# Performance work log

Measured on AMD Instinct MI355X. Metric: run time of the kernel, lower is better.

Reference implementation:

```python
import jax, jax.numpy as jnp
import numpy as np

B, S, D_IN, D_Q, D_V, H = 2, 2048, 1024, 1024, 1024, 16
HD_Q, HD_V = D_Q // H, D_V // H
SCALE = float(D_Q) ** 0.5  # source scales by sqrt(d_q), NOT sqrt(head_dim)


def setup_inputs() -> dict:
    key = jax.random.key(0)
    k1, k2, k3, k4, k5 = jax.random.split(key, 5)
    return {
        "x": jax.random.normal(k1, (B, S, D_IN), dtype=jnp.float32),
        "w_q": jax.random.normal(k2, (D_IN, D_Q), dtype=jnp.float32),
        "w_k": jax.random.normal(k3, (D_IN, D_Q), dtype=jnp.float32),
        "w_v": jax.random.normal(k4, (D_IN, D_V), dtype=jnp.float32),
        "W_o": jax.random.normal(k5, (D_IN, D_V), dtype=jnp.float32),
    }


def reference(x, w_q, w_k, w_v, W_o):
    b, s, _ = x.shape
    # projections: [b, s, d]
    q = x @ w_q
    k = x @ w_k
    v = x @ w_v
    # split heads -> [b, h, s, hd]
    Q = q.reshape(b, s, H, HD_Q).transpose(0, 2, 1, 3)
    K = k.reshape(b, s, H, HD_Q).transpose(0, 2, 1, 3)
    V = v.reshape(b, s, H, HD_V).transpose(0, 2, 1, 3)
    # full [b, h, s, s] score matrix (naive attention, as in source)
    scores = jnp.einsum("bhqd,bhkd->bhqk", Q, K)
    # FAITHFUL QUIRK: source applies softmax over dim=0 (batch axis)
    attn = jax.nn.softmax(scores / SCALE, axis=0)
    vals = jnp.einsum("bhqk,bhkd->bhqd", attn, V)
    vals = vals.transpose(0, 2, 1, 3).reshape(b, s, D_V)
    return vals @ W_o
```

## Files before the change

kernel.cpp:

```cpp
#include <hip/hip_runtime.h>


typedef _Float16 f16;
typedef __attribute__((ext_vector_type(8))) _Float16 f16x8;
typedef __attribute__((ext_vector_type(4))) _Float16 f16x4;
typedef __attribute__((ext_vector_type(4))) float f32x4;

#define MFMA16(a,b,c) __builtin_amdgcn_mfma_f32_16x16x32_f16(a,b,c,0,0,0)
#define GLD16(gp, lp) __builtin_amdgcn_global_load_lds(                         \
    (const __attribute__((address_space(1))) void*)(gp),                        \
    (__attribute__((address_space(3))) void*)(lp), 16, 0, 0)

__global__ __launch_bounds__(256) void convert_x(const float* __restrict__ x,
                                                 f16* __restrict__ xh, int n4) {
    int i = blockIdx.x * 256 + threadIdx.x;
    if (i >= n4) return;
    float4 v = ((const float4*)x)[i];
    f16x4 h;
    h[0] = (f16)v.x; h[1] = (f16)v.y; h[2] = (f16)v.z; h[3] = (f16)v.w;
    *(f16x4*)(xh + (long)i * 4) = h;
}

__global__ __launch_bounds__(256) void transpose_w(const float* __restrict__ w0, const float* __restrict__ w1,
                                                   const float* __restrict__ w2, const float* __restrict__ w3,
                                                   f16* __restrict__ o0, f16* __restrict__ o1,
                                                   f16* __restrict__ o2, f16* __restrict__ o3) {
    const float* w; f16* o;
    switch (blockIdx.z) {
        case 0: w = w0; o = o0; break;
        case 1: w = w1; o = o1; break;
        case 2: w = w2; o = o2; break;
        default: w = w3; o = o3; break;
    }
    __shared__ alignas(16) f16 t[64][72];
    const int tid = threadIdx.x;
    const int d0 = blockIdx.x * 64, j0 = blockIdx.y * 64;
    #pragma unroll
    for (int it = 0; it < 4; ++it) {
        int idx = it * 256 + tid;
        int row = idx >> 4, c4 = idx & 15;
        float4 v = *(const float4*)(w + (long)(d0 + row) * 1024 + j0 + c4 * 4);
        f16x4 h;
        h[0] = (f16)v.x; h[1] = (f16)v.y; h[2] = (f16)v.z; h[3] = (f16)v.w;
        *(f16x4*)&t[row][c4 * 4] = h;
    }
    __syncthreads();
    #pragma unroll
    for (int it = 0; it < 4; ++it) {
        int idx = it * 256 + tid;
        int jr = idx >> 4, d4 = idx & 15;
        f16x4 h;
        #pragma unroll
        for (int m = 0; m < 4; ++m) h[m] = t[d4 * 4 + m][jr];
        *(f16x4*)(o + (long)(j0 + jr) * 1024 + d0 + d4 * 4) = h;
    }
}

__global__ __launch_bounds__(256, 1) void gemm_qkv(const f16* __restrict__ A,
                                                   const f16* __restrict__ Wt,
                                                   f16* __restrict__ Qg,
                                                   f16* __restrict__ Kg,
                                                   f16* __restrict__ Vtg) {
    __shared__ alignas(16) f16 smem[16384];
    f16* As = smem;
    f16* Bs = smem + 8192;
    const int tid = threadIdx.x;
    const int wave = tid >> 6, lane = tid & 63;
    const int l15 = lane & 15, lq = lane >> 4;
    const int sw = l15 & 7;
    const int m0 = blockIdx.x * 128, n0 = blockIdx.y * 128;
    const int wr = (wave >> 1) * 64, wc = (wave & 1) * 64;
    const int r8 = lane >> 3;
    const int swc8 = ((lane & 7) ^ r8) * 8;

    f32x4 acc[4][4] = {};

    for (int kt = 0; kt < 16; ++kt) {
        __syncthreads();
        #pragma unroll
        for (int i = 0; i < 4; ++i) {
            GLD16(A  + (long)(m0 + wave * 32 + i * 8 + r8) * 1024 + kt * 64 + swc8, As + (wave * 32 + i * 8) * 64);
            GLD16(Wt + (long)(n0 + wave * 32 + i * 8 + r8) * 1024 + kt * 64 + swc8, Bs + (wave * 32 + i * 8) * 64);
        }
        __syncthreads();
        #pragma unroll
        for (int s2 = 0; s2 < 2; ++s2) {
            const int rc = ((s2 * 4 + lq) ^ sw) << 3;
            f16x8 af[4], bf[4];
            #pragma unroll
            for (int i = 0; i < 4; ++i) af[i] = *(const f16x8*)&As[(wr + i * 16 + l15) * 64 + rc];
            #pragma unroll
            for (int j = 0; j < 4; ++j) bf[j] = *(const f16x8*)&Bs[(wc + j * 16 + l15) * 64 + rc];
            #pragma unroll
            for (int i = 0; i < 4; ++i)
                #pragma unroll
                for (int j = 0; j < 4; ++j)
                    acc[i][j] = MFMA16(af[i], bf[j], acc[i][j]);
        }
    }

    const int sel = n0 >> 10;
    const int nb = n0 - (sel << 10);

    if (sel < 2) {
        f16* dst = sel == 0 ? Qg : Kg;
        const float qs = sel == 0 ? 0.045084219f : 1.0f;
        __syncthreads();
        #pragma unroll
        for (int i = 0; i < 4; ++i)
            #pragma unroll
            for (int j = 0; j < 4; ++j) {
                int row0 = wr + i * 16 + lq * 4;
                int colb = wc + j * 16 + l15;
                int chunk = colb >> 3, sub = colb & 7;
                #pragma unroll
                for (int r = 0; r < 4; ++r) {
                    int row = row0 + r;
                    smem[row * 128 + ((chunk ^ (row & 7)) << 3) + sub] = (f16)(acc[i][j][r] * qs);
                }
            }
        __syncthreads();
        #pragma unroll
        for (int e = 0; e < 8; ++e) {
            int id = e * 256 + tid;
            int row = id >> 4, c = id & 15;
            f16x8 v = *(const f16x8*)&smem[row * 128 + ((c ^ (row & 7)) << 3)];
            int gr = m0 + row, b = gr >> 11, s = gr & 2047;
            int gc = nb + c * 8, hh = gc >> 6, hd = gc & 63;
            *(f16x8*)(dst + (long)((b * 16 + hh) * 2048 + s) * 64 + hd) = v;
        }
    } else {
        #pragma unroll
        for (int i = 0; i < 4; ++i)
            #pragma unroll
            for (int j = 0; j < 4; ++j) {
                int gr0 = m0 + wr + i * 16 + lq * 4;
                int gc  = nb + wc + j * 16 + l15;
                int b = gr0 >> 11, s = gr0 & 2047;
                int hh = gc >> 6, hd = gc & 63;
                f16x4 v;
                #pragma unroll
                for (int r = 0; r < 4; ++r) v[r] = (f16)acc[i][j][r];
                *(f16x4*)(Vtg + (long)((b * 16 + hh) * 64 + hd) * 2048 + s) = v;
            }
    }
}

__global__ __launch_bounds__(256, 1) void gemm_out(const f16* __restrict__ A0,
                                                   const f16* __restrict__ A1,
                                                   const f16* __restrict__ Bt,
                                                   float* __restrict__ outp) {
    __shared__ alignas(16) f16 As[64][72];
    __shared__ alignas(16) f16 Bs[128][64];
    const int tid = threadIdx.x;
    const int wave = tid >> 6, lane = tid & 63;
    const int l15 = lane & 15, lq = lane >> 4;
    const int sw = l15 & 7;
    const int m0 = blockIdx.x * 64, n0 = blockIdx.y * 128;
    const int wr = (wave >> 1) * 32, wc = (wave & 1) * 64;
    const int r8 = lane >> 3;
    const int swc8 = ((lane & 7) ^ r8) * 8;

    f32x4 acc[2][4] = {};

    for (int kt = 0; kt < 16; ++kt) {
        __syncthreads();
        #pragma unroll
        for (int it = 0; it < 2; ++it) {
            int idx = it * 256 + tid;
            int row = idx >> 3, c = idx & 7;
            f16x8 a = *(const f16x8*)(A0 + (long)(m0 + row) * 1024 + kt * 64 + c * 8)
                    + *(const f16x8*)(A1 + (long)(m0 + row) * 1024 + kt * 64 + c * 8);
            *(f16x8*)&As[row][c * 8] = a;
        }
        #pragma unroll
        for (int i = 0; i < 4; ++i)
            GLD16(Bt + (long)(n0 + wave * 32 + i * 8 + r8) * 1024 + kt * 64 + swc8, &Bs[wave * 32 + i * 8][0]);
        __syncthreads();
        #pragma unroll
        for (int s2 = 0; s2 < 2; ++s2) {
            const int rc = ((s2 * 4 + lq) ^ sw) << 3;
            f16x8 af[2], bf[4];
            #pragma unroll
            for (int i = 0; i < 2; ++i) af[i] = *(const f16x8*)&As[wr + i * 16 + l15][s2 * 32 + lq * 8];
            #pragma unroll
            for (int j = 0; j < 4; ++j) bf[j] = *(const f16x8*)&Bs[wc + j * 16 + l15][rc];
            #pragma unroll
            for (int i = 0; i < 2; ++i)
                #pragma unroll
                for (int j = 0; j < 4; ++j)
                    acc[i][j] = MFMA16(af[i], bf[j], acc[i][j]);
        }
    }

    #pragma unroll
    for (int i = 0; i < 2; ++i)
        #pragma unroll
        for (int j = 0; j < 4; ++j) {
            int gr0 = m0 + wr + i * 16 + lq * 4;
            int gc  = n0 + wc + j * 16 + l15;
            #pragma unroll
            for (int r = 0; r < 4; ++r)
                outp[(long)(gr0 + r) * 1024 + gc] = acc[i][j][r];
        }
}

__global__ __launch_bounds__(128, 2) void attention_kernel(const f16* __restrict__ Qg,
                                                           const f16* __restrict__ Kg,
                                                           const f16* __restrict__ Vtg,
                                                           f16* __restrict__ vals0,
                                                           f16* __restrict__ vals1) {
    __shared__ alignas(16) f16 Ks [2][64][64];
    __shared__ alignas(16) f16 Vts[2][64][64];
    __shared__ alignas(16) f16 Ps [2][32][64];
    const int tid = threadIdx.x;
    const int wave = tid >> 6, lane = tid & 63;
    const int l15 = lane & 15, lq = lane >> 4;
    const int sw = l15 & 7;

    const int bid = blockIdx.x;
    const int xcd = bid & 7, sl = bid >> 3;
    const int h  = xcd * 2 + (sl & 1);
    const int qt = (sl >> 1) & 31, ks = sl >> 6;
    const int q0 = qt * 64, kt0 = ks * 16;
    f16* vals = ks ? vals1 : vals0;
    const int qr = q0 + wave * 32;

    f16x8 qfr[2][2][2];
    #pragma unroll
    for (int b2 = 0; b2 < 2; ++b2)
        #pragma unroll
        for (int qq = 0; qq < 2; ++qq)
            #pragma unroll
            for (int s2 = 0; s2 < 2; ++s2)
                qfr[b2][qq][s2] = *(const f16x8*)(Qg + (long)((b2 * 16 + h) * 2048 + qr + qq * 16 + l15) * 64
                                                  + s2 * 32 + lq * 8);

    f32x4 acc[2][2][4] = {};

    const int r8 = lane >> 3;
    const int swc8 = ((lane & 7) ^ r8) * 8;
    const f16* kb0 = Kg  + (long)(h * 2048 + kt0 * 64) * 64 + r8 * 64 + swc8;
    const f16* kb1 = kb0 + (long)16 * 2048 * 64;
    const f16* vb0 = Vtg + (long)(h * 64 + r8) * 2048 + kt0 * 64 + swc8;
    const f16* vb1 = vb0 + (long)16 * 64 * 2048;

    for (int kt = 0; kt < 16; ++kt) {
        __syncthreads();
        if (wave == 0) {
            const f16* g0 = kb0 + kt * 4096;
            const f16* g1 = kb1 + kt * 4096;
            #pragma unroll
            for (int i = 0; i < 8; ++i) GLD16(g0 + i * 512, &Ks[0][0][0] + i * 512);
            #pragma unroll
            for (int i = 0; i < 8; ++i) GLD16(g1 + i * 512, &Ks[1][0][0] + i * 512);
        } else {
            const f16* g0 = vb0 + kt * 64;
            const f16* g1 = vb1 + kt * 64;
            #pragma unroll
            for (int i = 0; i < 8; ++i) GLD16(g0 + (long)i * 8 * 2048, &Vts[0][0][0] + i * 512);
            #pragma unroll
            for (int i = 0; i < 8; ++i) GLD16(g1 + (long)i * 8 * 2048, &Vts[1][0][0] + i * 512);
        }
        __syncthreads();

        f16x4 pp0[2][4], pp1[2][4];
        #pragma unroll
        for (int kf = 0; kf < 4; ++kf) {
            f32x4 S0[2] = {}, S1[2] = {};
            #pragma unroll
            for (int s2 = 0; s2 < 2; ++s2) {
                const int rc = ((s2 * 4 + lq) ^ sw) << 3;
                f16x8 a0 = *(const f16x8*)&Ks[0][kf * 16 + l15][rc];
                f16x8 a1 = *(const f16x8*)&Ks[1][kf * 16 + l15][rc];
                #pragma unroll
                for (int qq = 0; qq < 2; ++qq) {
                    S0[qq] = MFMA16(a0, qfr[0][qq][s2], S0[qq]);
                    S1[qq] = MFMA16(a1, qfr[1][qq][s2], S1[qq]);
                }
            }
            #pragma unroll
            for (int qq = 0; qq < 2; ++qq)
                #pragma unroll
                for (int r = 0; r < 4; ++r) {
                    float e = __builtin_amdgcn_exp2f(S1[qq][r] - S0[qq][r]);
                    float p = __builtin_amdgcn_rcpf(1.0f + e);
                    pp0[qq][kf][r] = (f16)p;
                    pp1[qq][kf][r] = (f16)(1.0f - p);
                }
        }

        const int pwsub = (lq & 1) << 2;
        #pragma unroll
        for (int pb = 0; pb < 2; ++pb) {
            #pragma unroll
            for (int qq = 0; qq < 2; ++qq)
                #pragma unroll
                for (int kf = 0; kf < 4; ++kf)
                    *(f16x4*)&Ps[wave][qq * 16 + l15][(((2 * kf + (lq >> 1)) ^ sw) << 3) + pwsub]
                        = pb ? pp1[qq][kf] : pp0[qq][kf];
            #pragma unroll
            for (int s2 = 0; s2 < 2; ++s2) {
                const int rc = ((s2 * 4 + lq) ^ sw) << 3;
                f16x8 pf[2], vf[4];
                #pragma unroll
                for (int qq = 0; qq < 2; ++qq)
                    pf[qq] = *(const f16x8*)&Ps[wave][qq * 16 + l15][rc];
                #pragma unroll
                for (int hf = 0; hf < 4; ++hf)
                    vf[hf] = *(const f16x8*)&Vts[pb][hf * 16 + l15][rc];
                #pragma unroll
                for (int qq = 0; qq < 2; ++qq)
                    #pragma unroll
                    for (int hf = 0; hf < 4; ++hf)
                        acc[pb][qq][hf] = MFMA16(pf[qq], vf[hf], acc[pb][qq][hf]);
            }
        }
    }

    #pragma unroll
    for (int b2 = 0; b2 < 2; ++b2)
        #pragma unroll
        for (int qq = 0; qq < 2; ++qq)
            #pragma unroll
            for (int hf = 0; hf < 4; ++hf)
                #pragma unroll
                for (int r = 0; r < 4; ++r)
                    vals[(long)(b2 * 2048 + qr + qq * 16 + lq * 4 + r) * 1024 + h * 64 + hf * 16 + l15]
                        = (f16)acc[b2][qq][hf][r];
}

extern "C" void kernel_launch(void* const* d_in, const int* in_sizes, int n_in,
                              void* d_out, int out_size, void* d_ws, size_t ws_size,
                              hipStream_t stream) {
    const float* x  = (const float*)d_in[0];
    const float* wq = (const float*)d_in[1];
    const float* wk = (const float*)d_in[2];
    const float* wv = (const float*)d_in[3];
    const float* wo = (const float*)d_in[4];

    char* ws = (char*)d_ws;
    f16* xh    = (f16*)(ws);
    f16* wqT   = (f16*)(ws + 8388608);
    f16* wkT   = (f16*)(ws + 10485760);
    f16* wvT   = (f16*)(ws + 12582912);
    f16* woT   = (f16*)(ws + 14680064);
    f16* Qg    = (f16*)(ws + 16777216);
    f16* Kg    = (f16*)(ws + 25165824);
    f16* Vtg   = (f16*)(ws + 33554432);
    f16* vals1 = (f16*)(ws + 41943040);
    f16* vals0 = xh;
    (void)ws_size; (void)in_sizes; (void)n_in; (void)out_size;

    convert_x<<<4096, 256, 0, stream>>>(x, xh, (2 * 2048 * 1024) / 4);
    transpose_w<<<dim3(16, 16, 4), 256, 0, stream>>>(wq, wk, wv, wo, wqT, wkT, wvT, woT);

    gemm_qkv<<<dim3(32, 24), 256, 0, stream>>>(xh, wqT, Qg, Kg, Vtg);

    attention_kernel<<<1024, 128, 0, stream>>>(Qg, Kg, Vtg, vals0, vals1);

    gemm_out<<<dim3(64, 8), 256, 0, stream>>>(vals0, vals1, woT, (float*)d_out);
}
```

Measured before the change: 195.8 us.

## Double-buffer attention K/V tiles, widen attention blocks, fuse prep kernels

The attention kernel moves to 256-thread blocks covering 128 query rows, so K/V tiles in LDS are shared by four waves instead of two. It also double-buffers the K/V tiles so the next tile's global-to-LDS load is issued while the current tile is computed, leaving one barrier per iteration instead of two. Separately, the x conversion and weight transpose kernels are merged into one launch to save a kernel launch. The cost is double the LDS per block, which may lower occupancy.

```diff
diff --git a/kernel.cpp b/kernel.cpp
--- a/kernel.cpp
+++ b/kernel.cpp
@@ -11,30 +11,31 @@
     (const __attribute__((address_space(1))) void*)(gp),                        \
     (__attribute__((address_space(3))) void*)(lp), 16, 0, 0)
 
-__global__ __launch_bounds__(256) void convert_x(const float* __restrict__ x,
-                                                 f16* __restrict__ xh, int n4) {
-    int i = blockIdx.x * 256 + threadIdx.x;
-    if (i >= n4) return;
-    float4 v = ((const float4*)x)[i];
-    f16x4 h;
-    h[0] = (f16)v.x; h[1] = (f16)v.y; h[2] = (f16)v.z; h[3] = (f16)v.w;
-    *(f16x4*)(xh + (long)i * 4) = h;
-}
-
-__global__ __launch_bounds__(256) void transpose_w(const float* __restrict__ w0, const float* __restrict__ w1,
-                                                   const float* __restrict__ w2, const float* __restrict__ w3,
-                                                   f16* __restrict__ o0, f16* __restrict__ o1,
-                                                   f16* __restrict__ o2, f16* __restrict__ o3) {
+__global__ __launch_bounds__(256) void prep(const float* __restrict__ x,
+                                            const float* __restrict__ w0, const float* __restrict__ w1,
+                                            const float* __restrict__ w2, const float* __restrict__ w3,
+                                            f16* __restrict__ xh,
+                                            f16* __restrict__ o0, f16* __restrict__ o1,
+                                            f16* __restrict__ o2, f16* __restrict__ o3) {
+    const int bb = blockIdx.x;
+    const int tid = threadIdx.x;
+    if (bb >= 1024) {
+        int i = (bb - 1024) * 256 + tid;
+        float4 v = ((const float4*)x)[i];
+        f16x4 h;
+        h[0] = (f16)v.x; h[1] = (f16)v.y; h[2] = (f16)v.z; h[3] = (f16)v.w;
+        *(f16x4*)(xh + (long)i * 4) = h;
+        return;
+    }
     const float* w; f16* o;
-    switch (blockIdx.z) {
+    switch (bb & 3) {
         case 0: w = w0; o = o0; break;
         case 1: w = w1; o = o1; break;
         case 2: w = w2; o = o2; break;
         default: w = w3; o = o3; break;
     }
     __shared__ alignas(16) f16 t[64][72];
-    const int tid = threadIdx.x;
-    const int d0 = blockIdx.x * 64, j0 = blockIdx.y * 64;
+    const int d0 = ((bb >> 2) & 15) * 64, j0 = (bb >> 6) * 64;
     #pragma unroll
     for (int it = 0; it < 4; ++it) {
         int idx = it * 256 + tid;
@@ -205,14 +206,14 @@
         }
 }
 
-__global__ __launch_bounds__(128, 2) void attention_kernel(const f16* __restrict__ Qg,
+__global__ __launch_bounds__(256, 2) void attention_kernel(const f16* __restrict__ Qg,
                                                            const f16* __restrict__ Kg,
                                                            const f16* __restrict__ Vtg,
                                                            f16* __restrict__ vals0,
                                                            f16* __restrict__ vals1) {
-    __shared__ alignas(16) f16 Ks [2][64][64];
-    __shared__ alignas(16) f16 Vts[2][64][64];
-    __shared__ alignas(16) f16 Ps [2][32][64];
+    __shared__ alignas(16) f16 Ks [2][2][64][64];
+    __shared__ alignas(16) f16 Vts[2][2][64][64];
+    __shared__ alignas(16) f16 Ps [4][32][64];
     const int tid = threadIdx.x;
     const int wave = tid >> 6, lane = tid & 63;
     const int l15 = lane & 15, lq = lane >> 4;
@@ -221,8 +222,8 @@
     const int bid = blockIdx.x;
     const int xcd = bid & 7, sl = bid >> 3;
     const int h  = xcd * 2 + (sl & 1);
-    const int qt = (sl >> 1) & 31, ks = sl >> 6;
-    const int q0 = qt * 64, kt0 = ks * 16;
+    const int qt = (sl >> 1) & 15, ks = sl >> 5;
+    const int q0 = qt * 128, kt0 = ks * 16;
     f16* vals = ks ? vals1 : vals0;
     const int qr = q0 + wave * 32;
 
@@ -238,31 +239,31 @@
 
     f32x4 acc[2][2][4] = {};
 
+    const int tb = wave & 1;
     const int r8 = lane >> 3;
     const int swc8 = ((lane & 7) ^ r8) * 8;
-    const f16* kb0 = Kg  + (long)(h * 2048 + kt0 * 64) * 64 + r8 * 64 + swc8;
-    const f16* kb1 = kb0 + (long)16 * 2048 * 64;
-    const f16* vb0 = Vtg + (long)(h * 64 + r8) * 2048 + kt0 * 64 + swc8;
-    const f16* vb1 = vb0 + (long)16 * 64 * 2048;
-
+    const f16* kbase = Kg  + (long)((tb * 16 + h) * 2048 + kt0 * 64) * 64 + r8 * 64 + swc8;
+    const f16* vbase = Vtg + (long)((tb * 16 + h) * 64 + r8) * 2048 + kt0 * 64 + swc8;
+
+    auto stage = [&](int kt, int buf) {
+        if (wave < 2) {
+            const f16* g = kbase + kt * 4096;
+            f16* l = &Ks[buf][tb][0][0];
+            #pragma unroll
+            for (int i = 0; i < 8; ++i) GLD16(g + i * 512, l + i * 512);
+        } else {
+            const f16* g = vbase + kt * 64;
+            f16* l = &Vts[buf][tb][0][0];
+            #pragma unroll
+            for (int i = 0; i < 8; ++i) GLD16(g + (long)i * 8 * 2048, l + i * 512);
+        }
+    };
+
+    stage(0, 0);
     for (int kt = 0; kt < 16; ++kt) {
-        __syncthreads();
-        if (wave == 0) {
-            const f16* g0 = kb0 + kt * 4096;
-            const f16* g1 = kb1 + kt * 4096;
-            #pragma unroll
-            for (int i = 0; i < 8; ++i) GLD16(g0 + i * 512, &Ks[0][0][0] + i * 512);
-            #pragma unroll
-            for (int i = 0; i < 8; ++i) GLD16(g1 + i * 512, &Ks[1][0][0] + i * 512);
-        } else {
-            const f16* g0 = vb0 + kt * 64;
-            const f16* g1 = vb1 + kt * 64;
-            #pragma unroll
-            for (int i = 0; i < 8; ++i) GLD16(g0 + (long)i * 8 * 2048, &Vts[0][0][0] + i * 512);
-            #pragma unroll
-            for (int i = 0; i < 8; ++i) GLD16(g1 + (long)i * 8 * 2048, &Vts[1][0][0] + i * 512);
-        }
-        __syncthreads();
+        const int cur = kt & 1;
+        __syncthreads();
+        if (kt < 15) stage(kt + 1, cur ^ 1);
 
         f16x4 pp0[2][4], pp1[2][4];
         #pragma unroll
@@ -271,8 +272,8 @@
             #pragma unroll
             for (int s2 = 0; s2 < 2; ++s2) {
                 const int rc = ((s2 * 4 + lq) ^ sw) << 3;
-                f16x8 a0 = *(const f16x8*)&Ks[0][kf * 16 + l15][rc];
-                f16x8 a1 = *(const f16x8*)&Ks[1][kf * 16 + l15][rc];
+                f16x8 a0 = *(const f16x8*)&Ks[cur][0][kf * 16 + l15][rc];
+                f16x8 a1 = *(const f16x8*)&Ks[cur][1][kf * 16 + l15][rc];
                 #pragma unroll
                 for (int qq = 0; qq < 2; ++qq) {
                     S0[qq] = MFMA16(a0, qfr[0][qq][s2], S0[qq]);
@@ -308,7 +309,7 @@
                     pf[qq] = *(const f16x8*)&Ps[wave][qq * 16 + l15][rc];
                 #pragma unroll
                 for (int hf = 0; hf < 4; ++hf)
-                    vf[hf] = *(const f16x8*)&Vts[pb][hf * 16 + l15][rc];
+                    vf[hf] = *(const f16x8*)&Vts[cur][pb][hf * 16 + l15][rc];
                 #pragma unroll
                 for (int qq = 0; qq < 2; ++qq)
                     #pragma unroll
@@ -352,12 +353,11 @@
     f16* vals0 = xh;
     (void)ws_size; (void)in_sizes; (void)n_in; (void)out_size;
 
-    convert_x<<<4096, 256, 0, stream>>>(x, xh, (2 * 2048 * 1024) / 4);
-    transpose_w<<<dim3(16, 16, 4), 256, 0, stream>>>(wq, wk, wv, wo, wqT, wkT, wvT, woT);
+    prep<<<5120, 256, 0, stream>>>(x, wq, wk, wv, wo, xh, wqT, wkT, wvT, woT);
 
     gemm_qkv<<<dim3(32, 24), 256, 0, stream>>>(xh, wqT, Qg, Kg, Vtg);
 
-    attention_kernel<<<1024, 128, 0, stream>>>(Qg, Kg, Vtg, vals0, vals1);
+    attention_kernel<<<512, 256, 0, stream>>>(Qg, Kg, Vtg, vals0, vals1);
 
     gemm_out<<<dim3(64, 8), 256, 0, stream>>>(vals0, vals1, woT, (float*)d_out);
 }
```

Result: faster. 187.4 us (-4.3%).
